# Optimization experiments

Measured on AMD Instinct MI355X. Metric: run time of the kernel, lower is better.

Reference implementation:

```python
import jax, jax.numpy as jnp
import numpy as np

N, E, F_IN, HID, HEADS, B = 50000, 800000, 128, 128, 2, 256
EPS = 1e-5
NEG_SLOPE = 0.2


def gat_conv(x, src, dst, W, a_src, a_dst, b, heads, out_c, concat):
    n = x.shape[0]
    h = (x @ W).reshape(n, heads, out_c)            # [N,H,C]
    alpha_src = jnp.sum(h * a_src, axis=-1)          # [N,H]
    alpha_dst = jnp.sum(h * a_dst, axis=-1)          # [N,H]
    e = jax.nn.leaky_relu(alpha_src[src] + alpha_dst[dst], NEG_SLOPE)  # [E2,H]
    # segment softmax over incoming edges per destination node
    emax = jax.ops.segment_max(e, dst, num_segments=n)
    ex = jnp.exp(e - emax[dst])
    denom = jax.ops.segment_sum(ex, dst, num_segments=n)
    alpha = ex / denom[dst]                          # [E2,H]
    msg = h[src] * alpha[:, :, None]                 # [E2,H,C]
    out = jax.ops.segment_sum(msg, dst, num_segments=n)  # [N,H,C]
    if concat:
        out = out.reshape(n, heads * out_c)
    else:
        out = out.mean(axis=1)
    return out + b


def batchnorm_eval(x, gamma, beta, mean, var):
    return gamma * (x - mean) * jax.lax.rsqrt(var + EPS) + beta


def setup_inputs() -> dict:
    key = jax.random.key(0)
    ks = jax.random.split(key, 16)
    x = jax.random.normal(ks[0], (N, F_IN), dtype=jnp.float32)
    edge_index = jax.random.randint(ks[1], (2, E), 0, N, dtype=jnp.int64)
    batch = (jnp.arange(N, dtype=jnp.int64) * B) // N  # sorted, every graph non-empty
    s1 = 1.0 / np.sqrt(F_IN)
    s2 = 1.0 / np.sqrt(HEADS * HID)
    return {
        "x": x,
        "edge_index": edge_index,
        "batch": batch,
        "W1": jax.random.normal(ks[2], (F_IN, HEADS * HID), dtype=jnp.float32) * s1,
        "a_src1": jax.random.normal(ks[3], (HEADS, HID), dtype=jnp.float32) * s1,
        "a_dst1": jax.random.normal(ks[4], (HEADS, HID), dtype=jnp.float32) * s1,
        "b1": jnp.zeros((HEADS * HID,), dtype=jnp.float32),
        "gamma1": jnp.ones((HEADS * HID,), dtype=jnp.float32),
        "beta1": jnp.zeros((HEADS * HID,), dtype=jnp.float32),
        "rm1": jax.random.normal(ks[5], (HEADS * HID,), dtype=jnp.float32) * 0.1,
        "rv1": jax.random.uniform(ks[6], (HEADS * HID,), dtype=jnp.float32, minval=0.5, maxval=1.5),
        "W2": jax.random.normal(ks[7], (HEADS * HID, HID), dtype=jnp.float32) * s2,
        "a_src2": jax.random.normal(ks[8], (1, HID), dtype=jnp.float32) * s2,
        "a_dst2": jax.random.normal(ks[9], (1, HID), dtype=jnp.float32) * s2,
        "b2": jnp.zeros((HID,), dtype=jnp.float32),
        "gamma2": jnp.ones((HID,), dtype=jnp.float32),
        "beta2": jnp.zeros((HID,), dtype=jnp.float32),
        "rm2": jax.random.normal(ks[10], (HID,), dtype=jnp.float32) * 0.1,
        "rv2": jax.random.uniform(ks[11], (HID,), dtype=jnp.float32, minval=0.5, maxval=1.5),
    }


def reference(x, edge_index, batch, W1, a_src1, a_dst1, b1, gamma1, beta1, rm1, rv1,
              W2, a_src2, a_dst2, b2, gamma2, beta2, rm2, rv2):
    n = x.shape[0]
    # PyG GATConv adds self-loops by default
    loops = jnp.arange(n, dtype=edge_index.dtype)
    src = jnp.concatenate([edge_index[0], loops])
    dst = jnp.concatenate([edge_index[1], loops])

    h = gat_conv(x, src, dst, W1, a_src1, a_dst1, b1, HEADS, HID, concat=True)
    h = jax.nn.relu(batchnorm_eval(h, gamma1, beta1, rm1, rv1))  # dropout = identity (eval)

    h = gat_conv(h, src, dst, W2, a_src2, a_dst2, b2, 1, HID, concat=False)
    h = jax.nn.relu(batchnorm_eval(h, gamma2, beta2, rm2, rv2))

    # global max pool over graphs
    h_D = jax.ops.segment_max(h, batch, num_segments=B)  # [B, HID]
    return h_D
```

## Files before the change

### kernel.cpp

```cpp
#include <hip/hip_runtime.h>
#include <hip/hip_bf16.h>
#include <math.h>

#define NEG_SLOPE 0.2f
#define EPSBN 1e-5f

typedef __attribute__((ext_vector_type(8))) short bf16x8;
typedef __attribute__((ext_vector_type(4))) float f32x4;

__device__ __forceinline__ float bfu2f(unsigned u_lo16) { return __uint_as_float(u_lo16 << 16); }
__device__ __forceinline__ unsigned short f2bf(float f) {
    return __bfloat16_as_ushort(__float2bfloat16(f));
}
__device__ __forceinline__ void splitf(float v, unsigned short &h, unsigned short &l) {
    __hip_bfloat16 hb = __float2bfloat16(v);
    float r = v - __bfloat162float(hb);
    h = __bfloat16_as_ushort(hb);
    l = __bfloat16_as_ushort(__float2bfloat16(r));
}

__global__ void precompute_v(const float* __restrict__ W1, const float* __restrict__ as1,
                             const float* __restrict__ ad1, float* __restrict__ vsd)
{
    int k = threadIdx.x;
    if (k >= 128) return;
    float v0 = 0.f, v1 = 0.f, v2 = 0.f, v3 = 0.f;
    const float* wr = W1 + (size_t)k * 256;
    for (int c = 0; c < 128; ++c) {
        float wa = wr[c], wb = wr[128 + c];
        v0 += wa * as1[c];  v1 += wb * as1[128 + c];
        v2 += wa * ad1[c];  v3 += wb * ad1[128 + c];
    }
    vsd[k] = v0; vsd[128 + k] = v1; vsd[256 + k] = v2; vsd[384 + k] = v3;
}

__global__ __launch_bounds__(256) void split_x_attn(
    const float* __restrict__ X, const float* __restrict__ vsd,
    unsigned short* __restrict__ Xh,
    float* __restrict__ asrc, float* __restrict__ adst, int Nn)
{
    int n = (int)((blockIdx.x * blockDim.x + threadIdx.x) >> 6);
    int lane = threadIdx.x & 63;
    if (n >= Nn) return;
    float2 xv = *(const float2*)(X + (size_t)n * 128 + lane * 2);
    unsigned short hh[2] = {f2bf(xv.x), f2bf(xv.y)};
    *(unsigned*)(Xh + (size_t)n * 128 + lane * 2) = *(unsigned*)hh;
    int k = lane * 2;
    float p0 = xv.x * vsd[k]       + xv.y * vsd[k + 1];
    float p1 = xv.x * vsd[128 + k] + xv.y * vsd[129 + k];
    float p2 = xv.x * vsd[256 + k] + xv.y * vsd[257 + k];
    float p3 = xv.x * vsd[384 + k] + xv.y * vsd[385 + k];
    for (int off = 32; off; off >>= 1) {
        p0 += __shfl_xor(p0, off); p1 += __shfl_xor(p1, off);
        p2 += __shfl_xor(p2, off); p3 += __shfl_xor(p3, off);
    }
    if (lane == 0) {
        asrc[n * 2] = p0; asrc[n * 2 + 1] = p1;
        adst[n * 2] = p2; adst[n * 2 + 1] = p3;
    }
}

__global__ void split_w_both(const float* __restrict__ W1, const float* __restrict__ W2,
                             unsigned short* __restrict__ w1th, unsigned short* __restrict__ w1tl,
                             unsigned short* __restrict__ w2th, unsigned short* __restrict__ w2tl)
{
    int idx = blockIdx.x * blockDim.x + threadIdx.x;
    if (idx < 32768) {
        int nn = idx >> 7, k = idx & 127;
        unsigned short h, l; splitf(W1[(size_t)k * 256 + nn], h, l);
        w1th[idx] = h; w1tl[idx] = l;
    } else if (idx < 65536) {
        int j = idx - 32768;
        int nn = j >> 8, k = j & 255;
        unsigned short h, l; splitf(W2[(size_t)k * 128 + nn], h, l);
        w2th[j] = h; w2tl[j] = l;
    }
}

__global__ void count_edges(const int* __restrict__ ei, int E, int Nn,
                            int* __restrict__ counts, int* __restrict__ erank)
{
    int e = blockIdx.x * blockDim.x + threadIdx.x;
    int E2 = E + Nn;
    if (e >= E2) return;
    int dst = (e < E) ? ei[E + e] : (e - E);
    erank[e] = atomicAdd(&counts[dst], 1);
}

__global__ __launch_bounds__(256) void scan_block(
    const int* __restrict__ counts, int* __restrict__ offs, int* __restrict__ bsum, int Nn)
{
    __shared__ int s[256];
    int i = blockIdx.x * 256 + threadIdx.x;
    int v = (i < Nn) ? counts[i] : 0;
    s[threadIdx.x] = v;
    __syncthreads();
    for (int off = 1; off < 256; off <<= 1) {
        int t = (threadIdx.x >= off) ? s[threadIdx.x - off] : 0;
        __syncthreads();
        s[threadIdx.x] += t;
        __syncthreads();
    }
    if (i < Nn) offs[i] = s[threadIdx.x] - v;
    if (threadIdx.x == 255) bsum[blockIdx.x] = s[255];
}

__global__ __launch_bounds__(256) void scan_tops(int* __restrict__ bsum, int* __restrict__ boff, int nb)
{
    __shared__ int s[256];
    int v = (threadIdx.x < nb) ? bsum[threadIdx.x] : 0;
    s[threadIdx.x] = v;
    __syncthreads();
    for (int off = 1; off < 256; off <<= 1) {
        int t = (threadIdx.x >= off) ? s[threadIdx.x - off] : 0;
        __syncthreads();
        s[threadIdx.x] += t;
        __syncthreads();
    }
    if (threadIdx.x < nb) boff[threadIdx.x] = s[threadIdx.x] - v;
}

__global__ void add_offsets(int* __restrict__ offs, const int* __restrict__ boff, int Nn, int E2)
{
    int i = blockIdx.x * blockDim.x + threadIdx.x;
    if (i < Nn) offs[i] += boff[i >> 8];
    if (i == 0) offs[Nn] = E2;
}

__global__ void fill_edges(const int* __restrict__ ei, int E, int Nn,
                           const int* __restrict__ offs, const int* __restrict__ erank,
                           int* __restrict__ esrc)
{
    int e = blockIdx.x * blockDim.x + threadIdx.x;
    int E2 = E + Nn;
    if (e >= E2) return;
    int src, dst;
    if (e < E) { src = ei[e]; dst = ei[E + e]; }
    else       { src = e - E; dst = e - E; }
    esrc[offs[dst] + erank[e]] = src;
}

__device__ __forceinline__ void fma8(float wA, uint4 hv, float acc[8])
{
    acc[0] = fmaf(wA, bfu2f(hv.x & 0xffff), acc[0]);
    acc[1] = fmaf(wA, __uint_as_float(hv.x & 0xffff0000u), acc[1]);
    acc[2] = fmaf(wA, bfu2f(hv.y & 0xffff), acc[2]);
    acc[3] = fmaf(wA, __uint_as_float(hv.y & 0xffff0000u), acc[3]);
    acc[4] = fmaf(wA, bfu2f(hv.z & 0xffff), acc[4]);
    acc[5] = fmaf(wA, __uint_as_float(hv.z & 0xffff0000u), acc[5]);
    acc[6] = fmaf(wA, bfu2f(hv.w & 0xffff), acc[6]);
    acc[7] = fmaf(wA, __uint_as_float(hv.w & 0xffff0000u), acc[7]);
}

__device__ __forceinline__ void fma8x2(float wa, float wb, uint4 hv,
                                       float a0[8], float a1[8])
{
    float f;
    f = bfu2f(hv.x & 0xffff);                 a0[0]=fmaf(wa,f,a0[0]); a1[0]=fmaf(wb,f,a1[0]);
    f = __uint_as_float(hv.x & 0xffff0000u);  a0[1]=fmaf(wa,f,a0[1]); a1[1]=fmaf(wb,f,a1[1]);
    f = bfu2f(hv.y & 0xffff);                 a0[2]=fmaf(wa,f,a0[2]); a1[2]=fmaf(wb,f,a1[2]);
    f = __uint_as_float(hv.y & 0xffff0000u);  a0[3]=fmaf(wa,f,a0[3]); a1[3]=fmaf(wb,f,a1[3]);
    f = bfu2f(hv.z & 0xffff);                 a0[4]=fmaf(wa,f,a0[4]); a1[4]=fmaf(wb,f,a1[4]);
    f = __uint_as_float(hv.z & 0xffff0000u);  a0[5]=fmaf(wa,f,a0[5]); a1[5]=fmaf(wb,f,a1[5]);
    f = bfu2f(hv.w & 0xffff);                 a0[6]=fmaf(wa,f,a0[6]); a1[6]=fmaf(wb,f,a1[6]);
    f = __uint_as_float(hv.w & 0xffff0000u);  a0[7]=fmaf(wa,f,a0[7]); a1[7]=fmaf(wb,f,a1[7]);
}

__device__ __forceinline__ void gather1h(
    int sj, float w, int nc, int sub,
    const char* __restrict__ hb_c, float acc[8])
{
    for (int t = 0; t < nc; t += 4) {
        int e = t + sub;
        int sA = __shfl(sj, e);
        float wA = __shfl(w, e);
        uint4 hv = *(const uint4*)(hb_c + sA * 256);
        fma8(wA, hv, acc);
    }
}

__device__ __forceinline__ void gatherx(
    int sj, float w0, float w1, int nc, int sub,
    const char* __restrict__ hb_c, float a0[8], float a1[8])
{
    for (int t = 0; t < nc; t += 4) {
        int e = t + sub;
        int sA = __shfl(sj, e);
        float wa = __shfl(w0, e);
        float wb = __shfl(w1, e);
        uint4 hv = *(const uint4*)(hb_c + sA * 256);
        fma8x2(wa, wb, hv, a0, a1);
    }
}

__global__ __launch_bounds__(256) void spmm_x(
    const unsigned short* __restrict__ xh, const float* __restrict__ asrc,
    const float* __restrict__ adst, const int* __restrict__ offs,
    const int* __restrict__ esrc,
    unsigned short* __restrict__ xth, int Nn)
{
    int d = (int)((blockIdx.x * blockDim.x + threadIdx.x) >> 6);
    int lane = threadIdx.x & 63;
    if (d >= Nn) return;
    int beg = offs[d], end = offs[d + 1];
    int deg = end - beg;
    float ad0 = adst[d * 2], ad1 = adst[d * 2 + 1];
    const int sub = lane >> 4;
    const int cgrp = lane & 15;
    const char* hb_c = (const char*)xh + cgrp * 16;
    float a0[8] = {}, a1[8] = {};

    if (deg <= 64) {
        int sj = 0; float e0 = -1e30f, e1 = -1e30f;
        if (lane < deg) {
            sj = esrc[beg + lane];
            float2 av = *(const float2*)(asrc + (size_t)sj * 2);
            e0 = av.x + ad0; e0 = e0 > 0.f ? e0 : NEG_SLOPE * e0;
            e1 = av.y + ad1; e1 = e1 > 0.f ? e1 : NEG_SLOPE * e1;
        }
        float m0 = e0, m1 = e1;
        for (int off = 32; off; off >>= 1) {
            m0 = fmaxf(m0, __shfl_xor(m0, off));
            m1 = fmaxf(m1, __shfl_xor(m1, off));
        }
        float p0 = (lane < deg) ? expf(e0 - m0) : 0.f;
        float p1 = (lane < deg) ? expf(e1 - m1) : 0.f;
        float s0 = p0, s1 = p1;
        for (int off = 32; off; off >>= 1) {
            s0 += __shfl_xor(s0, off);
            s1 += __shfl_xor(s1, off);
        }
        float w0 = p0 * (1.f / s0), w1 = p1 * (1.f / s1);
        gatherx(sj, w0, w1, deg, sub, hb_c, a0, a1);
    } else {
        float m0 = -1e30f, m1 = -1e30f;
        for (int j = beg + lane; j < end; j += 64) {
            int s = esrc[j];
            float2 av = *(const float2*)(asrc + (size_t)s * 2);
            float e0 = av.x + ad0; e0 = e0 > 0.f ? e0 : NEG_SLOPE * e0;
            float e1 = av.y + ad1; e1 = e1 > 0.f ? e1 : NEG_SLOPE * e1;
            m0 = fmaxf(m0, e0); m1 = fmaxf(m1, e1);
        }
        for (int off = 32; off; off >>= 1) {
            m0 = fmaxf(m0, __shfl_xor(m0, off));
            m1 = fmaxf(m1, __shfl_xor(m1, off));
        }
        float s0 = 0.f, s1 = 0.f;
        for (int j = beg + lane; j < end; j += 64) {
            int s = esrc[j];
            float2 av = *(const float2*)(asrc + (size_t)s * 2);
            float e0 = av.x + ad0; e0 = e0 > 0.f ? e0 : NEG_SLOPE * e0;
            float e1 = av.y + ad1; e1 = e1 > 0.f ? e1 : NEG_SLOPE * e1;
            s0 += expf(e0 - m0); s1 += expf(e1 - m1);
        }
        for (int off = 32; off; off >>= 1) {
            s0 += __shfl_xor(s0, off);
            s1 += __shfl_xor(s1, off);
        }
        float rd0 = 1.f / s0, rd1 = 1.f / s1;
        for (int base = beg; base < end; base += 64) {
            int nc = end - base; if (nc > 64) nc = 64;
            int sj = 0; float w0 = 0.f, w1 = 0.f;
            if (lane < nc) {
                sj = esrc[base + lane];
                float2 av = *(const float2*)(asrc + (size_t)sj * 2);
                float e0 = av.x + ad0; e0 = e0 > 0.f ? e0 : NEG_SLOPE * e0;
                float e1 = av.y + ad1; e1 = e1 > 0.f ? e1 : NEG_SLOPE * e1;
                w0 = expf(e0 - m0) * rd0;
                w1 = expf(e1 - m1) * rd1;
            }
            gatherx(sj, w0, w1, nc, sub, hb_c, a0, a1);
        }
    }
#pragma unroll
    for (int i = 0; i < 8; ++i) {
        a0[i] += __shfl_xor(a0[i], 32); a0[i] += __shfl_xor(a0[i], 16);
        a1[i] += __shfl_xor(a1[i], 32); a1[i] += __shfl_xor(a1[i], 16);
    }
    if (lane < 16) {
        int cl = cgrp * 8;
        unsigned short h0[8], h1[8];
#pragma unroll
        for (int i = 0; i < 8; ++i) { h0[i] = f2bf(a0[i]); h1[i] = f2bf(a1[i]); }
        size_t rb = (size_t)d * 256;
        *(uint4*)(xth + rb + cl)       = *(uint4*)&h0[0];
        *(uint4*)(xth + rb + 128 + cl) = *(uint4*)&h1[0];
    }
}

__global__ __launch_bounds__(256) void gemm_bn_split(
    const unsigned short* __restrict__ Ah,
    const unsigned short* __restrict__ Bth, const unsigned short* __restrict__ Btl,
    const float* __restrict__ bias, const float* __restrict__ gamma,
    const float* __restrict__ beta, const float* __restrict__ rm,
    const float* __restrict__ rv,
    unsigned short* __restrict__ Ch, unsigned short* __restrict__ Cl, int M)
{
    __shared__ unsigned short smem[3][128][32];
    const int tid = threadIdx.x;
    const int lane = tid & 63;
    const int wave = tid >> 6;
    const int fr = lane & 15, g = lane >> 4;
    const int wr = (wave >> 1) * 64, wc = (wave & 1) * 64;
    const int rowBase = blockIdx.x * 128, colBase = blockIdx.y * 128;

    f32x4 acc[4][4] = {};

    for (int kk = 0; kk < 128; kk += 32) {
#pragma unroll
        for (int i = 0; i < 2; ++i) {
            int idx = tid + 256 * i;
            int r = idx >> 2, c = (idx & 3) * 8;
            int grow = rowBase + r;
            uint4 va_h = make_uint4(0, 0, 0, 0);
            if (grow < M) va_h = *(const uint4*)(Ah + (size_t)grow * 256 + colBase + kk + c);
            *(uint4*)&smem[0][r][c] = va_h;
            int gcol = colBase + r;
            *(uint4*)&smem[1][r][c] = *(const uint4*)(Bth + (size_t)gcol * 128 + kk + c);
            *(uint4*)&smem[2][r][c] = *(const uint4*)(Btl + (size_t)gcol * 128 + kk + c);
        }
        __syncthreads();

        bf16x8 ah[4], bh[4], bl[4];
#pragma unroll
        for (int m = 0; m < 4; ++m)
            ah[m] = *(const bf16x8*)&smem[0][wr + m * 16 + fr][g * 8];
#pragma unroll
        for (int n = 0; n < 4; ++n) {
            bh[n] = *(const bf16x8*)&smem[1][wc + n * 16 + fr][g * 8];
            bl[n] = *(const bf16x8*)&smem[2][wc + n * 16 + fr][g * 8];
        }
#pragma unroll
        for (int m = 0; m < 4; ++m)
#pragma unroll
            for (int n = 0; n < 4; ++n) {
                acc[m][n] = __builtin_amdgcn_mfma_f32_16x16x32_bf16(ah[m], bh[n], acc[m][n], 0, 0, 0);
                acc[m][n] = __builtin_amdgcn_mfma_f32_16x16x32_bf16(ah[m], bl[n], acc[m][n], 0, 0, 0);
            }
        __syncthreads();
    }

    {
        float bi[4], ga[4], bb[4], mu[4], iv[4];
#pragma unroll
        for (int n = 0; n < 4; ++n) {
            int c = colBase + wc + n * 16 + fr;
            bi[n] = bias[c]; ga[n] = gamma[c]; bb[n] = beta[c];
            mu[n] = rm[c];   iv[n] = rsqrtf(rv[c] + EPSBN);
        }
#pragma unroll
        for (int m = 0; m < 4; ++m)
#pragma unroll
            for (int n = 0; n < 4; ++n)
#pragma unroll
                for (int j = 0; j < 4; ++j) {
                    float v = acc[m][n][j] + bi[n];
                    v = ga[n] * (v - mu[n]) * iv[n] + bb[n];
                    acc[m][n][j] = fmaxf(v, 0.f);
                }
    }

    float* Cs = (float*)&smem[0][0][0];
    const int rl_w = (wr >> 6) * 16;
#pragma unroll
    for (int m = 0; m < 4; ++m) {
        __syncthreads();
#pragma unroll
        for (int n = 0; n < 4; ++n)
#pragma unroll
            for (int j = 0; j < 4; ++j)
                Cs[(rl_w + g * 4 + j) * 132 + wc + n * 16 + fr] = acc[m][n][j];
        __syncthreads();
        int rl = tid >> 3, c16 = (tid & 7) * 16;
        int grow = rowBase + (rl >> 4) * 64 + m * 16 + (rl & 15);
        if (grow < M) {
            unsigned short th[16], tl[16];
#pragma unroll
            for (int i = 0; i < 16; ++i) splitf(Cs[rl * 132 + c16 + i], th[i], tl[i]);
            size_t ob = (size_t)grow * 256 + colBase + c16;
            *(uint4*)(Ch + ob)     = *(uint4*)&th[0];
            *(uint4*)(Ch + ob + 8) = *(uint4*)&th[8];
            *(uint4*)(Cl + ob)     = *(uint4*)&tl[0];
            *(uint4*)(Cl + ob + 8) = *(uint4*)&tl[8];
        }
    }
}

__global__ __launch_bounds__(256) void gemm_bf16_split_attn(
    const unsigned short* __restrict__ Ah, const unsigned short* __restrict__ Al,
    const unsigned short* __restrict__ Bth, const unsigned short* __restrict__ Btl,
    unsigned short* __restrict__ Cb,
    const float* __restrict__ aSrc, const float* __restrict__ aDst,
    float* __restrict__ asrcOut, float* __restrict__ adstOut,
    int M, int N, int K, int heads)
{
    __shared__ unsigned short smem[4][128][32];
    const int tid = threadIdx.x;
    const int lane = tid & 63;
    const int wave = tid >> 6;
    const int fr = lane & 15, g = lane >> 4;
    const int wr = (wave >> 1) * 64, wc = (wave & 1) * 64;
    const int rowBase = blockIdx.x * 128, colBase = blockIdx.y * 128;

    f32x4 acc[4][4] = {};

    for (int kk = 0; kk < K; kk += 32) {
#pragma unroll
        for (int i = 0; i < 2; ++i) {
            int idx = tid + 256 * i;
            int r = idx >> 2, c = (idx & 3) * 8;
            int grow = rowBase + r;
            uint4 va_h, va_l;
            if (grow < M) {
                va_h = *(const uint4*)(Ah + (size_t)grow * K + kk + c);
                va_l = *(const uint4*)(Al + (size_t)grow * K + kk + c);
            } else {
                va_h = make_uint4(0, 0, 0, 0); va_l = make_uint4(0, 0, 0, 0);
            }
            *(uint4*)&smem[0][r][c] = va_h;
            *(uint4*)&smem[1][r][c] = va_l;
            int gcol = colBase + r;
            *(uint4*)&smem[2][r][c] = *(const uint4*)(Bth + (size_t)gcol * K + kk + c);
            *(uint4*)&smem[3][r][c] = *(const uint4*)(Btl + (size_t)gcol * K + kk + c);
        }
        __syncthreads();

        bf16x8 ah[4], al[4], bh[4], bl[4];
#pragma unroll
        for (int m = 0; m < 4; ++m) {
            ah[m] = *(const bf16x8*)&smem[0][wr + m * 16 + fr][g * 8];
            al[m] = *(const bf16x8*)&smem[1][wr + m * 16 + fr][g * 8];
        }
#pragma unroll
        for (int n = 0; n < 4; ++n) {
            bh[n] = *(const bf16x8*)&smem[2][wc + n * 16 + fr][g * 8];
            bl[n] = *(const bf16x8*)&smem[3][wc + n * 16 + fr][g * 8];
        }
#pragma unroll
        for (int m = 0; m < 4; ++m)
#pragma unroll
            for (int n = 0; n < 4; ++n) {
                acc[m][n] = __builtin_amdgcn_mfma_f32_16x16x32_bf16(ah[m], bh[n], acc[m][n], 0, 0, 0);
                acc[m][n] = __builtin_amdgcn_mfma_f32_16x16x32_bf16(ah[m], bl[n], acc[m][n], 0, 0, 0);
                acc[m][n] = __builtin_amdgcn_mfma_f32_16x16x32_bf16(al[m], bh[n], acc[m][n], 0, 0, 0);
            }
        __syncthreads();
    }

    {
        const int head = colBase >> 7;
        float avs[4], avd[4];
#pragma unroll
        for (int n = 0; n < 4; ++n) {
            int col = colBase + wc + n * 16 + fr;
            avs[n] = aSrc[col]; avd[n] = aDst[col];
        }
#pragma unroll
        for (int m = 0; m < 4; ++m) {
            float ps[4], pd[4];
#pragma unroll
            for (int j = 0; j < 4; ++j) {
                ps[j] = acc[m][0][j] * avs[0] + acc[m][1][j] * avs[1]
                      + acc[m][2][j] * avs[2] + acc[m][3][j] * avs[3];
                pd[j] = acc[m][0][j] * avd[0] + acc[m][1][j] * avd[1]
                      + acc[m][2][j] * avd[2] + acc[m][3][j] * avd[3];
            }
#pragma unroll
            for (int off = 8; off; off >>= 1)
#pragma unroll
                for (int j = 0; j < 4; ++j) {
                    ps[j] += __shfl_xor(ps[j], off);
                    pd[j] += __shfl_xor(pd[j], off);
                }
            if (fr == 0) {
#pragma unroll
                for (int j = 0; j < 4; ++j) {
                    int grow = rowBase + wr + m * 16 + g * 4 + j;
                    if (grow < M) {
                        atomicAdd(asrcOut + (size_t)grow * heads + head, ps[j]);
                        atomicAdd(adstOut + (size_t)grow * heads + head, pd[j]);
                    }
                }
            }
        }
    }

    float* Cs = (float*)&smem[0][0][0];
    const int rl_w = (wr >> 6) * 16;
#pragma unroll
    for (int m = 0; m < 4; ++m) {
        __syncthreads();
#pragma unroll
        for (int n = 0; n < 4; ++n)
#pragma unroll
            for (int j = 0; j < 4; ++j)
                Cs[(rl_w + g * 4 + j) * 132 + wc + n * 16 + fr] = acc[m][n][j];
        __syncthreads();
        int rl = tid >> 3, c16 = (tid & 7) * 16;
        int grow = rowBase + (rl >> 4) * 64 + m * 16 + (rl & 15);
        if (grow < M) {
            unsigned short tmp[16];
#pragma unroll
            for (int i = 0; i < 16; ++i) tmp[i] = f2bf(Cs[rl * 132 + c16 + i]);
            *(uint4*)(Cb + (size_t)grow * N + colBase + c16)     = *(uint4*)&tmp[0];
            *(uint4*)(Cb + (size_t)grow * N + colBase + c16 + 8) = *(uint4*)&tmp[8];
        }
    }
}

__global__ __launch_bounds__(256) void spmm2(
    const unsigned short* __restrict__ h2b, const float* __restrict__ asrc,
    const float* __restrict__ adst, const int* __restrict__ offs,
    const int* __restrict__ esrc,
    const float* __restrict__ b2, const float* __restrict__ gamma,
    const float* __restrict__ beta, const float* __restrict__ rm,
    const float* __restrict__ rv, float* __restrict__ x3, int Nn)
{
    int d = (int)((blockIdx.x * blockDim.x + threadIdx.x) >> 6);
    int lane = threadIdx.x & 63;
    if (d >= Nn) return;
    int beg = offs[d], end = offs[d + 1];
    int deg = end - beg;
    float ad = adst[d];
    const int sub = lane >> 4;
    const int cgrp = lane & 15;
    const char* hb_c = (const char*)h2b + cgrp * 16;
    float acc[8] = {};

    if (deg <= 64) {
        int sj = 0; float ev = -1e30f;
        if (lane < deg) {
            sj = esrc[beg + lane];
            float e = asrc[sj] + ad; ev = e > 0.f ? e : NEG_SLOPE * e;
        }
        float m = ev;
        for (int off = 32; off; off >>= 1) m = fmaxf(m, __shfl_xor(m, off));
        float p = (lane < deg) ? expf(ev - m) : 0.f;
        float s = p;
        for (int off = 32; off; off >>= 1) s += __shfl_xor(s, off);
        float w = p * (1.f / s);
        gather1h(sj, w, deg, sub, hb_c, acc);
    } else {
        float m = -1e30f;
        for (int j = beg + lane; j < end; j += 64) {
            int s = esrc[j];
            float e = asrc[s] + ad; e = e > 0.f ? e : NEG_SLOPE * e;
            m = fmaxf(m, e);
        }
        for (int off = 32; off; off >>= 1) m = fmaxf(m, __shfl_xor(m, off));
        float sd = 0.f;
        for (int j = beg + lane; j < end; j += 64) {
            int s = esrc[j];
            float e = asrc[s] + ad; e = e > 0.f ? e : NEG_SLOPE * e;
            sd += expf(e - m);
        }
        for (int off = 32; off; off >>= 1) sd += __shfl_xor(sd, off);
        float rd = 1.f / sd;
        for (int base = beg; base < end; base += 64) {
            int nc = end - base; if (nc > 64) nc = 64;
            int sj = 0; float wj = 0.f;
            if (lane < nc) {
                sj = esrc[base + lane];
                float e = asrc[sj] + ad; e = e > 0.f ? e : NEG_SLOPE * e;
                wj = expf(e - m) * rd;
            }
            gather1h(sj, wj, nc, sub, hb_c, acc);
        }
    }
#pragma unroll
    for (int i = 0; i < 8; ++i) {
        acc[i] += __shfl_xor(acc[i], 32);
        acc[i] += __shfl_xor(acc[i], 16);
    }
    if (lane < 16) {
        int cl = cgrp * 8;
        float vv[8];
#pragma unroll
        for (int i = 0; i < 8; ++i) {
            int c = cl + i;
            float v = acc[i] + b2[c];
            v = gamma[c] * (v - rm[c]) * rsqrtf(rv[c] + EPSBN) + beta[c];
            vv[i] = fmaxf(v, 0.f);
        }
        *(float4*)(x3 + (size_t)d * 128 + cl)     = make_float4(vv[0], vv[1], vv[2], vv[3]);
        *(float4*)(x3 + (size_t)d * 128 + cl + 4) = make_float4(vv[4], vv[5], vv[6], vv[7]);
    }
}

__global__ __launch_bounds__(128) void pool_max_graph(
    const float* __restrict__ x3, const int* __restrict__ bat,
    float* __restrict__ out, int Nn)
{
    int g = blockIdx.x;
    int c = threadIdx.x;
    int lo = 0, hi = Nn;
    while (lo < hi) { int mid = (lo + hi) >> 1; if (bat[mid] < g) lo = mid + 1; else hi = mid; }
    int beg = lo;
    hi = Nn;
    while (lo < hi) { int mid = (lo + hi) >> 1; if (bat[mid] < g + 1) lo = mid + 1; else hi = mid; }
    int end = lo;
    float acc = -1e30f;
    for (int n = beg; n < end; ++n)
        acc = fmaxf(acc, x3[(size_t)n * 128 + c]);
    out[(size_t)g * 128 + c] = acc;
}

extern "C" void kernel_launch(void* const* d_in, const int* in_sizes, int n_in,
                              void* d_out, int out_size, void* d_ws, size_t ws_size,
                              hipStream_t stream)
{
    const float* x   = (const float*)d_in[0];
    const int*   ei  = (const int*)d_in[1];
    const int*   bat = (const int*)d_in[2];
    const float* W1  = (const float*)d_in[3];
    const float* as1 = (const float*)d_in[4];
    const float* ad1 = (const float*)d_in[5];
    const float* b1  = (const float*)d_in[6];
    const float* g1  = (const float*)d_in[7];
    const float* be1 = (const float*)d_in[8];
    const float* rm1 = (const float*)d_in[9];
    const float* rv1 = (const float*)d_in[10];
    const float* W2  = (const float*)d_in[11];
    const float* as2 = (const float*)d_in[12];
    const float* ad2 = (const float*)d_in[13];
    const float* b2  = (const float*)d_in[14];
    const float* g2  = (const float*)d_in[15];
    const float* be2 = (const float*)d_in[16];
    const float* rm2 = (const float*)d_in[17];
    const float* rv2 = (const float*)d_in[18];
    float* out = (float*)d_out;

    const int Nn = in_sizes[0] / 128;
    const int E  = in_sizes[1] / 2;
    const int E2 = E + Nn;
    const int B  = out_size / 128;

    char* p = (char*)d_ws;
    size_t off = 0;
    auto alloc = [&](size_t bytes) -> void* {
        void* r = p + off;
        off = (off + bytes + 255) & ~(size_t)255;
        return r;
    };
    unsigned short* xh    = (unsigned short*)alloc((size_t)Nn * 128 * 2);
    unsigned short* w1th  = (unsigned short*)alloc(256 * 128 * 2);
    unsigned short* w1tl  = (unsigned short*)alloc(256 * 128 * 2);
    unsigned short* w2th  = (unsigned short*)alloc(128 * 256 * 2);
    unsigned short* w2tl  = (unsigned short*)alloc(128 * 256 * 2);
    unsigned short* xth   = (unsigned short*)alloc((size_t)Nn * 256 * 2);
    unsigned short* x2h   = (unsigned short*)alloc((size_t)Nn * 256 * 2);
    unsigned short* x2l   = (unsigned short*)alloc((size_t)Nn * 256 * 2);
    float*          vsd   = (float*)alloc(4 * 128 * 4);
    float*          asrc1 = (float*)alloc((size_t)Nn * 2 * 4);
    float*          adst1 = (float*)alloc((size_t)Nn * 2 * 4);
    float*          attnv = (float*)alloc((size_t)Nn * 2 * 4);
    float*          asrc2 = attnv;
    float*          adst2 = attnv + Nn;
    int*            counts= (int*)alloc((size_t)Nn * 4);
    int*            erank = (int*)alloc((size_t)E2 * 4);
    int*            offs  = (int*)alloc((size_t)(Nn + 1) * 4);
    int*            bsum  = (int*)alloc(256 * 4);
    int*            boff  = (int*)alloc(256 * 4);
    int*            esrc  = (int*)alloc((size_t)E2 * 4);
    float*          x3    = (float*)xth;
    unsigned short* h2b   = xh;

    const int nb = (Nn + 255) / 256;
    const int nwB = (Nn + 3) / 4;
    const int gmB = (Nn + 127) / 128;

    hipMemsetAsync(counts, 0, (size_t)Nn * 4, stream);
    hipMemsetAsync(attnv, 0, (size_t)Nn * 2 * 4, stream);

    precompute_v<<<1, 128, 0, stream>>>(W1, as1, ad1, vsd);
    split_x_attn<<<nwB, 256, 0, stream>>>(x, vsd, xh, asrc1, adst1, Nn);
    split_w_both<<<(65536 + 255) / 256, 256, 0, stream>>>(W1, W2, w1th, w1tl, w2th, w2tl);

    count_edges<<<(E2 + 255) / 256, 256, 0, stream>>>(ei, E, Nn, counts, erank);
    scan_block<<<nb, 256, 0, stream>>>(counts, offs, bsum, Nn);
    scan_tops<<<1, 256, 0, stream>>>(bsum, boff, nb);
    add_offsets<<<(Nn + 255) / 256, 256, 0, stream>>>(offs, boff, Nn, E2);
    fill_edges<<<(E2 + 255) / 256, 256, 0, stream>>>(ei, E, Nn, offs, erank, esrc);

    spmm_x<<<nwB, 256, 0, stream>>>(xh, asrc1, adst1, offs, esrc, xth, Nn);
    gemm_bn_split<<<dim3(gmB, 2), 256, 0, stream>>>(
        xth, w1th, w1tl, b1, g1, be1, rm1, rv1, x2h, x2l, Nn);

    gemm_bf16_split_attn<<<dim3(gmB, 1), 256, 0, stream>>>(
        x2h, x2l, w2th, w2tl, h2b, as2, ad2, asrc2, adst2, Nn, 128, 256, 1);
    spmm2<<<nwB, 256, 0, stream>>>(h2b, asrc2, adst2, offs, esrc,
                                   b2, g2, be2, rm2, rv2, x3, Nn);

    pool_max_graph<<<B, 128, 0, stream>>>(x3, bat, out, Nn);
}
```

Before: 267.2 us.

## Merge prep kernels, drop low-half split of layer-1 output, store final activations as bf16

Three preprocessing kernels (x split/attention, weight split, edge counting) are merged into one launch with block-range dispatch. The first GEMM now writes only the bf16 high half of its output, not a high/low pair. The second GEMM therefore drops the A-low operand and one of its three MFMAs per tile and is specialised to fixed sizes. The spmm2 output feeding the max-pool is stored as bf16 instead of fp32. Together these cut launches, memory traffic and MFMA work, at the cost of lower precision in the layer-2 input and the final pooled values.

Measured after the change: 249.6 us. 1.07x faster.

```diff
diff --git a/kernel.cpp b/kernel.cpp
--- a/kernel.cpp
+++ b/kernel.cpp
@@ -34,57 +34,57 @@
     vsd[k] = v0; vsd[128 + k] = v1; vsd[256 + k] = v2; vsd[384 + k] = v3;
 }
 
-__global__ __launch_bounds__(256) void split_x_attn(
+__global__ __launch_bounds__(256) void prep(
     const float* __restrict__ X, const float* __restrict__ vsd,
-    unsigned short* __restrict__ Xh,
-    float* __restrict__ asrc, float* __restrict__ adst, int Nn)
-{
-    int n = (int)((blockIdx.x * blockDim.x + threadIdx.x) >> 6);
-    int lane = threadIdx.x & 63;
-    if (n >= Nn) return;
-    float2 xv = *(const float2*)(X + (size_t)n * 128 + lane * 2);
-    unsigned short hh[2] = {f2bf(xv.x), f2bf(xv.y)};
-    *(unsigned*)(Xh + (size_t)n * 128 + lane * 2) = *(unsigned*)hh;
-    int k = lane * 2;
-    float p0 = xv.x * vsd[k]       + xv.y * vsd[k + 1];
-    float p1 = xv.x * vsd[128 + k] + xv.y * vsd[129 + k];
-    float p2 = xv.x * vsd[256 + k] + xv.y * vsd[257 + k];
-    float p3 = xv.x * vsd[384 + k] + xv.y * vsd[385 + k];
-    for (int off = 32; off; off >>= 1) {
-        p0 += __shfl_xor(p0, off); p1 += __shfl_xor(p1, off);
-        p2 += __shfl_xor(p2, off); p3 += __shfl_xor(p3, off);
-    }
-    if (lane == 0) {
-        asrc[n * 2] = p0; asrc[n * 2 + 1] = p1;
-        adst[n * 2] = p2; adst[n * 2 + 1] = p3;
-    }
-}
-
-__global__ void split_w_both(const float* __restrict__ W1, const float* __restrict__ W2,
-                             unsigned short* __restrict__ w1th, unsigned short* __restrict__ w1tl,
-                             unsigned short* __restrict__ w2th, unsigned short* __restrict__ w2tl)
-{
-    int idx = blockIdx.x * blockDim.x + threadIdx.x;
-    if (idx < 32768) {
-        int nn = idx >> 7, k = idx & 127;
-        unsigned short h, l; splitf(W1[(size_t)k * 256 + nn], h, l);
-        w1th[idx] = h; w1tl[idx] = l;
-    } else if (idx < 65536) {
-        int j = idx - 32768;
-        int nn = j >> 8, k = j & 255;
-        unsigned short h, l; splitf(W2[(size_t)k * 128 + nn], h, l);
-        w2th[j] = h; w2tl[j] = l;
-    }
-}
-
-__global__ void count_edges(const int* __restrict__ ei, int E, int Nn,
-                            int* __restrict__ counts, int* __restrict__ erank)
-{
-    int e = blockIdx.x * blockDim.x + threadIdx.x;
-    int E2 = E + Nn;
-    if (e >= E2) return;
-    int dst = (e < E) ? ei[E + e] : (e - E);
-    erank[e] = atomicAdd(&counts[dst], 1);
+    const float* __restrict__ W1, const float* __restrict__ W2,
+    const int* __restrict__ ei,
+    unsigned short* __restrict__ Xh, float* __restrict__ asrc, float* __restrict__ adst,
+    unsigned short* __restrict__ w1th, unsigned short* __restrict__ w1tl,
+    unsigned short* __restrict__ w2th, unsigned short* __restrict__ w2tl,
+    int* __restrict__ counts, int* __restrict__ erank,
+    int Nn, int E, int nwB, int countB)
+{
+    const int b = blockIdx.x;
+    const int tid = threadIdx.x;
+    if (b < nwB) {
+        int n = (int)((b * 256 + tid) >> 6);
+        int lane = tid & 63;
+        if (n >= Nn) return;
+        float2 xv = *(const float2*)(X + (size_t)n * 128 + lane * 2);
+        unsigned short hh[2] = {f2bf(xv.x), f2bf(xv.y)};
+        *(unsigned*)(Xh + (size_t)n * 128 + lane * 2) = *(unsigned*)hh;
+        int k = lane * 2;
+        float p0 = xv.x * vsd[k]       + xv.y * vsd[k + 1];
+        float p1 = xv.x * vsd[128 + k] + xv.y * vsd[129 + k];
+        float p2 = xv.x * vsd[256 + k] + xv.y * vsd[257 + k];
+        float p3 = xv.x * vsd[384 + k] + xv.y * vsd[385 + k];
+        for (int off = 32; off; off >>= 1) {
+            p0 += __shfl_xor(p0, off); p1 += __shfl_xor(p1, off);
+            p2 += __shfl_xor(p2, off); p3 += __shfl_xor(p3, off);
+        }
+        if (lane == 0) {
+            asrc[n * 2] = p0; asrc[n * 2 + 1] = p1;
+            adst[n * 2] = p2; adst[n * 2 + 1] = p3;
+        }
+    } else if (b < nwB + countB) {
+        int e = (b - nwB) * 256 + tid;
+        int E2 = E + Nn;
+        if (e >= E2) return;
+        int dst = (e < E) ? ei[E + e] : (e - E);
+        erank[e] = atomicAdd(&counts[dst], 1);
+    } else {
+        int idx = (b - nwB - countB) * 256 + tid;
+        if (idx < 32768) {
+            int nn = idx >> 7, k = idx & 127;
+            unsigned short h, l; splitf(W1[(size_t)k * 256 + nn], h, l);
+            w1th[idx] = h; w1tl[idx] = l;
+        } else if (idx < 65536) {
+            int j = idx - 32768;
+            int nn = j >> 8, k = j & 255;
+            unsigned short h, l; splitf(W2[(size_t)k * 128 + nn], h, l);
+            w2th[j] = h; w2tl[j] = l;
+        }
+    }
 }
 
 __global__ __launch_bounds__(256) void scan_block(
@@ -294,7 +294,7 @@
     const float* __restrict__ bias, const float* __restrict__ gamma,
     const float* __restrict__ beta, const float* __restrict__ rm,
     const float* __restrict__ rv,
-    unsigned short* __restrict__ Ch, unsigned short* __restrict__ Cl, int M)
+    unsigned short* __restrict__ Ch, int M)
 {
     __shared__ unsigned short smem[3][128][32];
     const int tid = threadIdx.x;
@@ -374,67 +374,55 @@
         int rl = tid >> 3, c16 = (tid & 7) * 16;
         int grow = rowBase + (rl >> 4) * 64 + m * 16 + (rl & 15);
         if (grow < M) {
-            unsigned short th[16], tl[16];
-#pragma unroll
-            for (int i = 0; i < 16; ++i) splitf(Cs[rl * 132 + c16 + i], th[i], tl[i]);
+            unsigned short th[16];
+#pragma unroll
+            for (int i = 0; i < 16; ++i) th[i] = f2bf(Cs[rl * 132 + c16 + i]);
             size_t ob = (size_t)grow * 256 + colBase + c16;
             *(uint4*)(Ch + ob)     = *(uint4*)&th[0];
             *(uint4*)(Ch + ob + 8) = *(uint4*)&th[8];
-            *(uint4*)(Cl + ob)     = *(uint4*)&tl[0];
-            *(uint4*)(Cl + ob + 8) = *(uint4*)&tl[8];
-        }
-    }
-}
-
-__global__ __launch_bounds__(256) void gemm_bf16_split_attn(
-    const unsigned short* __restrict__ Ah, const unsigned short* __restrict__ Al,
+        }
+    }
+}
+
+__global__ __launch_bounds__(256) void gemm_bf16_attn(
+    const unsigned short* __restrict__ Ah,
     const unsigned short* __restrict__ Bth, const unsigned short* __restrict__ Btl,
     unsigned short* __restrict__ Cb,
     const float* __restrict__ aSrc, const float* __restrict__ aDst,
-    float* __restrict__ asrcOut, float* __restrict__ adstOut,
-    int M, int N, int K, int heads)
-{
-    __shared__ unsigned short smem[4][128][32];
+    float* __restrict__ asrcOut, float* __restrict__ adstOut, int M)
+{
+    __shared__ unsigned short smem[3][128][32];
     const int tid = threadIdx.x;
     const int lane = tid & 63;
     const int wave = tid >> 6;
     const int fr = lane & 15, g = lane >> 4;
     const int wr = (wave >> 1) * 64, wc = (wave & 1) * 64;
-    const int rowBase = blockIdx.x * 128, colBase = blockIdx.y * 128;
+    const int rowBase = blockIdx.x * 128;
 
     f32x4 acc[4][4] = {};
 
-    for (int kk = 0; kk < K; kk += 32) {
+    for (int kk = 0; kk < 256; kk += 32) {
 #pragma unroll
         for (int i = 0; i < 2; ++i) {
             int idx = tid + 256 * i;
             int r = idx >> 2, c = (idx & 3) * 8;
             int grow = rowBase + r;
-            uint4 va_h, va_l;
-            if (grow < M) {
-                va_h = *(const uint4*)(Ah + (size_t)grow * K + kk + c);
-                va_l = *(const uint4*)(Al + (size_t)grow * K + kk + c);
-            } else {
-                va_h = make_uint4(0, 0, 0, 0); va_l = make_uint4(0, 0, 0, 0);
-            }
+            uint4 va_h = make_uint4(0, 0, 0, 0);
+            if (grow < M) va_h = *(const uint4*)(Ah + (size_t)grow * 256 + kk + c);
             *(uint4*)&smem[0][r][c] = va_h;
-            *(uint4*)&smem[1][r][c] = va_l;
-            int gcol = colBase + r;
-            *(uint4*)&smem[2][r][c] = *(const uint4*)(Bth + (size_t)gcol * K + kk + c);
-            *(uint4*)&smem[3][r][c] = *(const uint4*)(Btl + (size_t)gcol * K + kk + c);
-        }
-        __syncthreads();
-
-        bf16x8 ah[4], al[4], bh[4], bl[4];
-#pragma unroll
-        for (int m = 0; m < 4; ++m) {
+            *(uint4*)&smem[1][r][c] = *(const uint4*)(Bth + (size_t)r * 256 + kk + c);
+            *(uint4*)&smem[2][r][c] = *(const uint4*)(Btl + (size_t)r * 256 + kk + c);
+        }
+        __syncthreads();
+
+        bf16x8 ah[4], bh[4], bl[4];
+#pragma unroll
+        for (int m = 0; m < 4; ++m)
             ah[m] = *(const bf16x8*)&smem[0][wr + m * 16 + fr][g * 8];
-            al[m] = *(const bf16x8*)&smem[1][wr + m * 16 + fr][g * 8];
-        }
 #pragma unroll
         for (int n = 0; n < 4; ++n) {
-            bh[n] = *(const bf16x8*)&smem[2][wc + n * 16 + fr][g * 8];
-            bl[n] = *(const bf16x8*)&smem[3][wc + n * 16 + fr][g * 8];
+            bh[n] = *(const bf16x8*)&smem[1][wc + n * 16 + fr][g * 8];
+            bl[n] = *(const bf16x8*)&smem[2][wc + n * 16 + fr][g * 8];
         }
 #pragma unroll
         for (int m = 0; m < 4; ++m)
@@ -442,17 +430,15 @@
             for (int n = 0; n < 4; ++n) {
                 acc[m][n] = __builtin_amdgcn_mfma_f32_16x16x32_bf16(ah[m], bh[n], acc[m][n], 0, 0, 0);
                 acc[m][n] = __builtin_amdgcn_mfma_f32_16x16x32_bf16(ah[m], bl[n], acc[m][n], 0, 0, 0);
-                acc[m][n] = __builtin_amdgcn_mfma_f32_16x16x32_bf16(al[m], bh[n], acc[m][n], 0, 0, 0);
             }
         __syncthreads();
     }
 
     {
-        const int head = colBase >> 7;
         float avs[4], avd[4];
 #pragma unroll
         for (int n = 0; n < 4; ++n) {
-            int col = colBase + wc + n * 16 + fr;
+            int col = wc + n * 16 + fr;
             avs[n] = aSrc[col]; avd[n] = aDst[col];
         }
 #pragma unroll
@@ -477,8 +463,8 @@
                 for (int j = 0; j < 4; ++j) {
                     int grow = rowBase + wr + m * 16 + g * 4 + j;
                     if (grow < M) {
-                        atomicAdd(asrcOut + (size_t)grow * heads + head, ps[j]);
-                        atomicAdd(adstOut + (size_t)grow * heads + head, pd[j]);
+                        atomicAdd(asrcOut + grow, ps[j]);
+                        atomicAdd(adstOut + grow, pd[j]);
                     }
                 }
             }
@@ -502,8 +488,8 @@
             unsigned short tmp[16];
 #pragma unroll
             for (int i = 0; i < 16; ++i) tmp[i] = f2bf(Cs[rl * 132 + c16 + i]);
-            *(uint4*)(Cb + (size_t)grow * N + colBase + c16)     = *(uint4*)&tmp[0];
-            *(uint4*)(Cb + (size_t)grow * N + colBase + c16 + 8) = *(uint4*)&tmp[8];
+            *(uint4*)(Cb + (size_t)grow * 128 + c16)     = *(uint4*)&tmp[0];
+            *(uint4*)(Cb + (size_t)grow * 128 + c16 + 8) = *(uint4*)&tmp[8];
         }
     }
 }
@@ -514,7 +500,7 @@
     const int* __restrict__ esrc,
     const float* __restrict__ b2, const float* __restrict__ gamma,
     const float* __restrict__ beta, const float* __restrict__ rm,
-    const float* __restrict__ rv, float* __restrict__ x3, int Nn)
+    const float* __restrict__ rv, unsigned short* __restrict__ x3b, int Nn)
 {
     int d = (int)((blockIdx.x * blockDim.x + threadIdx.x) >> 6);
     int lane = threadIdx.x & 63;
@@ -574,21 +560,20 @@
     }
     if (lane < 16) {
         int cl = cgrp * 8;
-        float vv[8];
+        unsigned short hh[8];
 #pragma unroll
         for (int i = 0; i < 8; ++i) {
             int c = cl + i;
             float v = acc[i] + b2[c];
             v = gamma[c] * (v - rm[c]) * rsqrtf(rv[c] + EPSBN) + beta[c];
-            vv[i] = fmaxf(v, 0.f);
-        }
-        *(float4*)(x3 + (size_t)d * 128 + cl)     = make_float4(vv[0], vv[1], vv[2], vv[3]);
-        *(float4*)(x3 + (size_t)d * 128 + cl + 4) = make_float4(vv[4], vv[5], vv[6], vv[7]);
+            hh[i] = f2bf(fmaxf(v, 0.f));
+        }
+        *(uint4*)(x3b + (size_t)d * 128 + cl) = *(uint4*)&hh[0];
     }
 }
 
 __global__ __launch_bounds__(128) void pool_max_graph(
-    const float* __restrict__ x3, const int* __restrict__ bat,
+    const unsigned short* __restrict__ x3b, const int* __restrict__ bat,
     float* __restrict__ out, int Nn)
 {
     int g = blockIdx.x;
@@ -601,7 +586,7 @@
     int end = lo;
     float acc = -1e30f;
     for (int n = beg; n < end; ++n)
-        acc = fmaxf(acc, x3[(size_t)n * 128 + c]);
+        acc = fmaxf(acc, bfu2f((unsigned)x3b[(size_t)n * 128 + c]));
     out[(size_t)g * 128 + c] = acc;
 }
 
@@ -649,7 +634,6 @@
     unsigned short* w2tl  = (unsigned short*)alloc(128 * 256 * 2);
     unsigned short* xth   = (unsigned short*)alloc((size_t)Nn * 256 * 2);
     unsigned short* x2h   = (unsigned short*)alloc((size_t)Nn * 256 * 2);
-    unsigned short* x2l   = (unsigned short*)alloc((size_t)Nn * 256 * 2);
     float*          vsd   = (float*)alloc(4 * 128 * 4);
     float*          asrc1 = (float*)alloc((size_t)Nn * 2 * 4);
     float*          adst1 = (float*)alloc((size_t)Nn * 2 * 4);
@@ -662,21 +646,22 @@
     int*            bsum  = (int*)alloc(256 * 4);
     int*            boff  = (int*)alloc(256 * 4);
     int*            esrc  = (int*)alloc((size_t)E2 * 4);
-    float*          x3    = (float*)xth;
+    unsigned short* x3b   = xth;
     unsigned short* h2b   = xh;
 
     const int nb = (Nn + 255) / 256;
     const int nwB = (Nn + 3) / 4;
+    const int countB = (E2 + 255) / 256;
     const int gmB = (Nn + 127) / 128;
 
     hipMemsetAsync(counts, 0, (size_t)Nn * 4, stream);
     hipMemsetAsync(attnv, 0, (size_t)Nn * 2 * 4, stream);
 
     precompute_v<<<1, 128, 0, stream>>>(W1, as1, ad1, vsd);
-    split_x_attn<<<nwB, 256, 0, stream>>>(x, vsd, xh, asrc1, adst1, Nn);
-    split_w_both<<<(65536 + 255) / 256, 256, 0, stream>>>(W1, W2, w1th, w1tl, w2th, w2tl);
-
-    count_edges<<<(E2 + 255) / 256, 256, 0, stream>>>(ei, E, Nn, counts, erank);
+    prep<<<nwB + countB + 256, 256, 0, stream>>>(
+        x, vsd, W1, W2, ei, xh, asrc1, adst1,
+        w1th, w1tl, w2th, w2tl, counts, erank, Nn, E, nwB, countB);
+
     scan_block<<<nb, 256, 0, stream>>>(counts, offs, bsum, Nn);
     scan_tops<<<1, 256, 0, stream>>>(bsum, boff, nb);
     add_offsets<<<(Nn + 255) / 256, 256, 0, stream>>>(offs, boff, Nn, E2);
@@ -684,12 +669,12 @@
 
     spmm_x<<<nwB, 256, 0, stream>>>(xh, asrc1, adst1, offs, esrc, xth, Nn);
     gemm_bn_split<<<dim3(gmB, 2), 256, 0, stream>>>(
-        xth, w1th, w1tl, b1, g1, be1, rm1, rv1, x2h, x2l, Nn);
-
-    gemm_bf16_split_attn<<<dim3(gmB, 1), 256, 0, stream>>>(
-        x2h, x2l, w2th, w2tl, h2b, as2, ad2, asrc2, adst2, Nn, 128, 256, 1);
+        xth, w1th, w1tl, b1, g1, be1, rm1, rv1, x2h, Nn);
+
+    gemm_bf16_attn<<<gmB, 256, 0, stream>>>(
+        x2h, w2th, w2tl, h2b, as2, ad2, asrc2, adst2, Nn);
     spmm2<<<nwB, 256, 0, stream>>>(h2b, asrc2, adst2, offs, esrc,
-                                   b2, g2, be2, rm2, rv2, x3, Nn);
-
-    pool_max_graph<<<B, 128, 0, stream>>>(x3, bat, out, Nn);
-}
+                                   b2, g2, be2, rm2, rv2, x3b, Nn);
+
+    pool_max_graph<<<B, 128, 0, stream>>>(x3b, bat, out, Nn);
+}
```
